# Kernel optimization log

Hardware: AMD Instinct MI355X
Metric: run time of the kernel (lower is better)

The kernel has to match this reference:

```python
import jax, jax.numpy as jnp
import numpy as np

B, T, D_IN, D_H = 32, 2048, 256, 256


def setup_inputs() -> dict:
    key = jax.random.key(0)
    k1, k2, k3 = jax.random.split(key, 3)
    s_in = 1.0 / np.sqrt(D_IN)
    s_h = 1.0 / np.sqrt(D_H)
    return {
        "x": jax.random.normal(k1, (B, T, D_IN), dtype=jnp.float32),
        "h": jnp.zeros((B, D_H), dtype=jnp.float32),
        "W_in": jax.random.normal(k2, (D_IN, D_H), dtype=jnp.float32) * s_in,
        "b_in": jnp.zeros((D_H,), dtype=jnp.float32),
        "W_h": jax.random.normal(k3, (D_H, D_H), dtype=jnp.float32) * s_h,
        "b_h": jnp.zeros((D_H,), dtype=jnp.float32),
    }


def reference(x, h, W_in, b_in, W_h, b_h):
    # x: [B, T, D_in] (batch_first). Precompute input projection for all t
    # (mathematically identical, avoids T tiny GEMMs on x).
    x_proj = jnp.einsum("btd,dh->bth", x, W_in) + b_in  # [B, T, H]
    x_proj_t = jnp.swapaxes(x_proj, 0, 1)  # time-major [T, B, H]

    def step(h_prev, xp_t):
        h_new = jax.nn.relu(xp_t + h_prev @ W_h + b_h)  # [B, H]
        return h_new, h_new

    _, hs = jax.lax.scan(step, h, x_proj_t)  # hs: [T, B, H]
    return jnp.swapaxes(hs, 0, 1)  # [B, T, H]
```

## Files before the change

### kernel.cpp

```cpp
#include <hip/hip_runtime.h>

#define T_LEN 2048
#define DH 256
#define NCHUNK (T_LEN / 16)

typedef short short8 __attribute__((ext_vector_type(8)));
typedef float f32x4 __attribute__((ext_vector_type(4)));

__device__ __forceinline__ unsigned short f2bf(float f) {
  unsigned u = __builtin_bit_cast(unsigned, f);
  u += 0x7fffu + ((u >> 16) & 1u);
  return (unsigned short)(u >> 16);
}

#define STEP_BARRIER() do {                                 \
  asm volatile("s_waitcnt lgkmcnt(0)" ::: "memory");        \
  __builtin_amdgcn_s_barrier();                             \
  __builtin_amdgcn_sched_barrier(0);                        \
} while (0)

__global__ __launch_bounds__(256, 1) void xproj_gemm(
    const float* __restrict__ x, const float* __restrict__ W_in,
    const float* __restrict__ b_in, const float* __restrict__ b_h,
    float* __restrict__ out) {
  const int tid  = threadIdx.x;
  const int lane = tid & 63;
  const int w    = tid >> 6;
  const int l15  = lane & 15;
  const int lg   = lane >> 4;
  const int koff = lg * 8;
  const int m0   = blockIdx.x * 128;

  short8 Bf[4][8];
#pragma unroll
  for (int n = 0; n < 4; ++n) {
    const int c = 64 * w + 16 * n + l15;
#pragma unroll
    for (int kk = 0; kk < 8; ++kk) {
      short8 bf;
#pragma unroll
      for (int j = 0; j < 8; ++j)
        bf[j] = (short)f2bf(W_in[(32 * kk + koff + j) * DH + c]);
      Bf[n][kk] = bf;
    }
  }
  float bin[4];
#pragma unroll
  for (int n = 0; n < 4; ++n) {
    const int c = 64 * w + 16 * n + l15;
    bin[n] = b_in[c] + b_h[c];
  }

  for (int slab = 0; slab < 8; ++slab) {
    const float* xr = x + (size_t)(m0 + slab * 16 + l15) * DH;
    short8 A[8];
#pragma unroll
    for (int kk = 0; kk < 8; ++kk) {
      f32x4 v0 = *(const f32x4*)(xr + 32 * kk + koff);
      f32x4 v1 = *(const f32x4*)(xr + 32 * kk + koff + 4);
      short8 a;
      a[0] = f2bf(v0[0]); a[1] = f2bf(v0[1]); a[2] = f2bf(v0[2]); a[3] = f2bf(v0[3]);
      a[4] = f2bf(v1[0]); a[5] = f2bf(v1[1]); a[6] = f2bf(v1[2]); a[7] = f2bf(v1[3]);
      A[kk] = a;
    }
    f32x4 acc[4];
#pragma unroll
    for (int n = 0; n < 4; ++n) acc[n] = (f32x4){0.f, 0.f, 0.f, 0.f};
#pragma unroll
    for (int kk = 0; kk < 8; ++kk)
#pragma unroll
      for (int n = 0; n < 4; ++n)
        acc[n] = __builtin_amdgcn_mfma_f32_16x16x32_bf16(A[kk], Bf[n][kk], acc[n], 0, 0, 0);
#pragma unroll
    for (int n = 0; n < 4; ++n) {
      const int c = 64 * w + 16 * n + l15;
#pragma unroll
      for (int r = 0; r < 4; ++r)
        out[(size_t)(m0 + slab * 16 + lg * 4 + r) * DH + c] = acc[n][r] + bin[n];
    }
  }
}

__global__ __launch_bounds__(512, 2) void rnn_scan(
    const float* __restrict__ h0, const float* __restrict__ W_h,
    float* __restrict__ out) {
  __shared__ __align__(16) unsigned short hb[2][DH];

  const int tid  = threadIdx.x;
  const int lane = tid & 63;
  const int w    = tid >> 6;
  const int l15  = lane & 15;
  const int lg   = lane >> 4;
  const int koff = lg * 8;
  const int b    = blockIdx.x;
  float* outb = out + (size_t)b * T_LEN * DH;

  float xbA[32], xbB[32];

  auto ISSUE_XB = [&](int cc, float (&xb)[32]) {
    if (cc < NCHUNK && lane < 16) {
      const float* p = outb + (size_t)cc * 16 * DH + 32 * w + l15;
#pragma unroll
      for (int s = 0; s < 16; ++s) {
        xb[2 * s]     = p[(size_t)s * DH];
        xb[2 * s + 1] = p[(size_t)s * DH + 16];
      }
    }
  };

  ISSUE_XB(0, xbA);
  ISSUE_XB(1, xbB);

  short8 Bf[2][8];
#pragma unroll
  for (int n = 0; n < 2; ++n) {
    const int c = 32 * w + 16 * n + l15;
#pragma unroll
    for (int kk = 0; kk < 8; ++kk) {
      short8 bf;
#pragma unroll
      for (int j = 0; j < 8; ++j)
        bf[j] = (short)f2bf(W_h[(32 * kk + koff + j) * DH + c]);
      Bf[n][kk] = bf;
    }
  }

  if (tid < DH) hb[0][tid] = f2bf(h0[b * DH + tid]);
  __syncthreads();

  short8 A[8];
#pragma unroll
  for (int kk = 0; kk < 8; ++kk) A[kk] = (short8){0, 0, 0, 0, 0, 0, 0, 0};

  auto CHUNK = [&](int cc, float (&xb)[32]) {
    float* orow = outb + (size_t)cc * 16 * DH;
#pragma unroll
    for (int s = 0; s < 16; ++s) {
      const unsigned short* hbR = hb[s & 1];
      unsigned short* hbW = hb[(s + 1) & 1];
      if (l15 == 0) {
#pragma unroll
        for (int kk = 0; kk < 8; ++kk)
          A[kk] = *(const short8*)(hbR + 32 * kk + koff);
      }

      f32x4 ac[2][2];
#pragma unroll
      for (int n = 0; n < 2; ++n) {
        ac[n][0] = (f32x4){0.f, 0.f, 0.f, 0.f};
        ac[n][1] = (f32x4){0.f, 0.f, 0.f, 0.f};
      }
#pragma unroll
      for (int kk = 0; kk < 4; ++kk)
#pragma unroll
        for (int n = 0; n < 2; ++n)
          ac[n][0] = __builtin_amdgcn_mfma_f32_16x16x32_bf16(A[kk], Bf[n][kk], ac[n][0], 0, 0, 0);
#pragma unroll
      for (int kk = 4; kk < 8; ++kk)
#pragma unroll
        for (int n = 0; n < 2; ++n)
          ac[n][1] = __builtin_amdgcn_mfma_f32_16x16x32_bf16(A[kk], Bf[n][kk], ac[n][1], 0, 0, 0);

      if (lane < 16) {
        float v0 = (ac[0][0][0] + ac[0][1][0]) + xb[2 * s];
        float v1 = (ac[1][0][0] + ac[1][1][0]) + xb[2 * s + 1];
        v0 = fmaxf(v0, 0.0f);
        v1 = fmaxf(v1, 0.0f);
        hbW[32 * w + lane]      = f2bf(v0);
        hbW[32 * w + 16 + lane] = f2bf(v1);
        orow[(size_t)s * DH + 32 * w + lane]      = v0;
        orow[(size_t)s * DH + 32 * w + 16 + lane] = v1;
      }
      STEP_BARRIER();
    }
    ISSUE_XB(cc + 2, xb);
  };

  for (int c2 = 0; c2 < NCHUNK; c2 += 2) {
    CHUNK(c2, xbA);
    CHUNK(c2 + 1, xbB);
  }
}

extern "C" void kernel_launch(void* const* d_in, const int* in_sizes, int n_in,
                              void* d_out, int out_size, void* d_ws, size_t ws_size,
                              hipStream_t stream) {
  const float* x    = (const float*)d_in[0];
  const float* h0   = (const float*)d_in[1];
  const float* W_in = (const float*)d_in[2];
  const float* b_in = (const float*)d_in[3];
  const float* W_h  = (const float*)d_in[4];
  const float* b_h  = (const float*)d_in[5];
  float* out = (float*)d_out;

  hipLaunchKernelGGL(xproj_gemm, dim3(512), dim3(256), 0, stream, x, W_in, b_in, b_h, out);
  hipLaunchKernelGGL(rnn_scan, dim3(32), dim3(512), 0, stream, h0, W_h, out);
}
```

Before: 840.9 us.

## Batch 16 sequences per block in RNN scan to fill MFMA rows

```diff
diff --git a/kernel.cpp b/kernel.cpp
--- a/kernel.cpp
+++ b/kernel.cpp
@@ -2,7 +2,6 @@
 
 #define T_LEN 2048
 #define DH 256
-#define NCHUNK (T_LEN / 16)
 
 typedef short short8 __attribute__((ext_vector_type(8)));
 typedef float f32x4 __attribute__((ext_vector_type(4)));
@@ -84,33 +83,32 @@
 __global__ __launch_bounds__(512, 2) void rnn_scan(
     const float* __restrict__ h0, const float* __restrict__ W_h,
     float* __restrict__ out) {
-  __shared__ __align__(16) unsigned short hb[2][DH];
+  __shared__ __align__(16) unsigned short hb[2][16 * DH];
 
   const int tid  = threadIdx.x;
   const int lane = tid & 63;
   const int w    = tid >> 6;
   const int l15  = lane & 15;
   const int lg   = lane >> 4;
+  const int g    = blockIdx.x;
+
+  float* sp0[4];
+#pragma unroll
+  for (int r = 0; r < 4; ++r) {
+    const int m = 4 * lg + r;
+    sp0[r] = out + (size_t)(16 * g + m) * T_LEN * DH + 32 * w + l15;
+  }
+
+  float xq[4][8];
+#pragma unroll
+  for (int s = 0; s < 4; ++s)
+#pragma unroll
+    for (int n = 0; n < 2; ++n)
+#pragma unroll
+      for (int r = 0; r < 4; ++r)
+        xq[s][n * 4 + r] = sp0[r][(size_t)s * DH + 16 * n];
+
   const int koff = lg * 8;
-  const int b    = blockIdx.x;
-  float* outb = out + (size_t)b * T_LEN * DH;
-
-  float xbA[32], xbB[32];
-
-  auto ISSUE_XB = [&](int cc, float (&xb)[32]) {
-    if (cc < NCHUNK && lane < 16) {
-      const float* p = outb + (size_t)cc * 16 * DH + 32 * w + l15;
-#pragma unroll
-      for (int s = 0; s < 16; ++s) {
-        xb[2 * s]     = p[(size_t)s * DH];
-        xb[2 * s + 1] = p[(size_t)s * DH + 16];
-      }
-    }
-  };
-
-  ISSUE_XB(0, xbA);
-  ISSUE_XB(1, xbB);
-
   short8 Bf[2][8];
 #pragma unroll
   for (int n = 0; n < 2; ++n) {
@@ -125,61 +123,99 @@
     }
   }
 
-  if (tid < DH) hb[0][tid] = f2bf(h0[b * DH + tid]);
+  int aoff[8];
+#pragma unroll
+  for (int kk = 0; kk < 8; ++kk)
+    aoff[kk] = l15 * 512 + ((64 * kk + 16 * lg) ^ (l15 << 4));
+  int woff[8];
+#pragma unroll
+  for (int n = 0; n < 2; ++n)
+#pragma unroll
+    for (int r = 0; r < 4; ++r) {
+      const int m = 4 * lg + r;
+      woff[n * 4 + r] = m * 512 + ((64 * w + 32 * n + 2 * l15) ^ (m << 4));
+    }
+
+  {
+    const int m  = tid >> 5;
+    const int c0 = (tid & 31) * 8;
+    const float* hp = h0 + (size_t)(16 * g + m) * DH + c0;
+    short8 pk;
+#pragma unroll
+    for (int j = 0; j < 8; ++j) pk[j] = (short)f2bf(hp[j]);
+    *(short8*)((char*)hb + m * 512 + ((2 * c0) ^ (m << 4))) = pk;
+  }
   __syncthreads();
 
-  short8 A[8];
-#pragma unroll
-  for (int kk = 0; kk < 8; ++kk) A[kk] = (short8){0, 0, 0, 0, 0, 0, 0, 0};
-
-  auto CHUNK = [&](int cc, float (&xb)[32]) {
-    float* orow = outb + (size_t)cc * 16 * DH;
-#pragma unroll
-    for (int s = 0; s < 16; ++s) {
-      const unsigned short* hbR = hb[s & 1];
-      unsigned short* hbW = hb[(s + 1) & 1];
-      if (l15 == 0) {
-#pragma unroll
-        for (int kk = 0; kk < 8; ++kk)
-          A[kk] = *(const short8*)(hbR + 32 * kk + koff);
-      }
-
-      f32x4 ac[2][2];
-#pragma unroll
-      for (int n = 0; n < 2; ++n) {
-        ac[n][0] = (f32x4){0.f, 0.f, 0.f, 0.f};
-        ac[n][1] = (f32x4){0.f, 0.f, 0.f, 0.f};
-      }
-#pragma unroll
-      for (int kk = 0; kk < 4; ++kk)
-#pragma unroll
-        for (int n = 0; n < 2; ++n)
-          ac[n][0] = __builtin_amdgcn_mfma_f32_16x16x32_bf16(A[kk], Bf[n][kk], ac[n][0], 0, 0, 0);
-#pragma unroll
-      for (int kk = 4; kk < 8; ++kk)
-#pragma unroll
-        for (int n = 0; n < 2; ++n)
-          ac[n][1] = __builtin_amdgcn_mfma_f32_16x16x32_bf16(A[kk], Bf[n][kk], ac[n][1], 0, 0, 0);
-
-      if (lane < 16) {
-        float v0 = (ac[0][0][0] + ac[0][1][0]) + xb[2 * s];
-        float v1 = (ac[1][0][0] + ac[1][1][0]) + xb[2 * s + 1];
-        v0 = fmaxf(v0, 0.0f);
-        v1 = fmaxf(v1, 0.0f);
-        hbW[32 * w + lane]      = f2bf(v0);
-        hbW[32 * w + 16 + lane] = f2bf(v1);
-        orow[(size_t)s * DH + 32 * w + lane]      = v0;
-        orow[(size_t)s * DH + 32 * w + 16 + lane] = v1;
-      }
-      STEP_BARRIER();
-    }
-    ISSUE_XB(cc + 2, xb);
-  };
-
-  for (int c2 = 0; c2 < NCHUNK; c2 += 2) {
-    CHUNK(c2, xbA);
-    CHUNK(c2 + 1, xbB);
-  }
+  float* sp = (float*)sp0[0];
+  (void)sp;
+
+  const float* lp[4];
+#pragma unroll
+  for (int r = 0; r < 4; ++r) lp[r] = sp0[r] + 4 * DH;
+
+#define STEP(s, REFILL) do {                                                  \
+    const int rb_ = (s) & 1, wb_ = ((s) + 1) & 1;                             \
+    short8 A_[8];                                                             \
+    _Pragma("unroll")                                                         \
+    for (int kk = 0; kk < 8; ++kk)                                            \
+      A_[kk] = *(const short8*)((const char*)hb + rb_ * 8192 + aoff[kk]);     \
+    f32x4 ac_[2][2];                                                          \
+    _Pragma("unroll")                                                         \
+    for (int n = 0; n < 2; ++n) {                                             \
+      ac_[n][0] = (f32x4){0.f, 0.f, 0.f, 0.f};                                \
+      ac_[n][1] = (f32x4){0.f, 0.f, 0.f, 0.f};                                \
+    }                                                                         \
+    _Pragma("unroll")                                                         \
+    for (int kk = 0; kk < 4; ++kk)                                            \
+      _Pragma("unroll")                                                       \
+      for (int n = 0; n < 2; ++n)                                             \
+        ac_[n][0] = __builtin_amdgcn_mfma_f32_16x16x32_bf16(A_[kk], Bf[n][kk], ac_[n][0], 0, 0, 0); \
+    _Pragma("unroll")                                                         \
+    for (int kk = 4; kk < 8; ++kk)                                            \
+      _Pragma("unroll")                                                       \
+      for (int n = 0; n < 2; ++n)                                             \
+        ac_[n][1] = __builtin_amdgcn_mfma_f32_16x16x32_bf16(A_[kk], Bf[n][kk], ac_[n][1], 0, 0, 0); \
+                                                       \
+    f32x4 v_[2];                                                              \
+    _Pragma("unroll")                                                         \
+    for (int n = 0; n < 2; ++n)                                               \
+      _Pragma("unroll")                                                       \
+      for (int r = 0; r < 4; ++r)                                             \
+        v_[n][r] = fmaxf(ac_[n][0][r] + ac_[n][1][r] + xq[s][n * 4 + r], 0.f);\
+                                                  \
+    if (REFILL) {                                                             \
+      _Pragma("unroll")                                                       \
+      for (int n = 0; n < 2; ++n)                                             \
+        _Pragma("unroll")                                                     \
+        for (int r = 0; r < 4; ++r)                                           \
+          xq[s][n * 4 + r] = lp[r][(size_t)(s) * DH + 16 * n];                \
+    }                                                                         \
+              \
+    _Pragma("unroll")                                                         \
+    for (int n = 0; n < 2; ++n)                                               \
+      _Pragma("unroll")                                                       \
+      for (int r = 0; r < 4; ++r) {                                           \
+        *(unsigned short*)((char*)hb + wb_ * 8192 + woff[n * 4 + r]) =        \
+            f2bf(v_[n][r]);                                                   \
+        sp0[r][(size_t)(s) * DH + 16 * n] = v_[n][r];                         \
+      }                                                                       \
+    STEP_BARRIER();                                                           \
+  } while (0)
+
+  for (int it = 0; it < T_LEN / 4; ++it) {
+    const bool refill = (it + 1 < T_LEN / 4);
+    STEP(0, refill);
+    STEP(1, refill);
+    STEP(2, refill);
+    STEP(3, refill);
+#pragma unroll
+    for (int r = 0; r < 4; ++r) {
+      sp0[r] += 4 * DH;
+      lp[r]  += 4 * DH;
+    }
+  }
+#undef STEP
 }
 
 extern "C" void kernel_launch(void* const* d_in, const int* in_sizes, int n_in,
@@ -194,5 +230,5 @@
   float* out = (float*)d_out;
 
   hipLaunchKernelGGL(xproj_gemm, dim3(512), dim3(256), 0, stream, x, W_in, b_in, b_h, out);
-  hipLaunchKernelGGL(rnn_scan, dim3(32), dim3(512), 0, stream, h0, W_h, out);
-}
+  hipLaunchKernelGGL(rnn_scan, dim3(2), dim3(512), 0, stream, h0, W_h, out);
+}
```

New measurement: 1.640 ms. +95.0%, slower.
